# Optimization experiments

Measured on AMD Instinct MI355X. Metric: run time of the kernel, lower is better.

## Reference

```python
import math
import jax, jax.numpy as jnp
import numpy as np

H = 8  # h_heads (init kwarg)
D = 512  # d_hiddens
N, S = 4, 1024  # batch, seq (q == s assumed by the module's mask construction)
NEG = -1.0e9


def setup_inputs() -> dict:
    key = jax.random.key(0)
    ks = jax.random.split(key, 13)
    scale = 1.0 / math.sqrt(D)
    inp = {
        "queries_nqd": jax.random.normal(ks[0], (N, S, D), jnp.float32),
        "keys_nsd": jax.random.normal(ks[1], (N, S, D), jnp.float32),
        "values_nsd": jax.random.normal(ks[2], (N, S, D), jnp.float32),
        "prefix_len_n": jax.random.randint(ks[3], (N,), 0, S),
        "Wq": jax.random.normal(ks[4], (D, D), jnp.float32) * scale,
        "bq": jnp.zeros((D,), jnp.float32),
        "Wk": jax.random.normal(ks[5], (D, D), jnp.float32) * scale,
        "bk": jnp.zeros((D,), jnp.float32),
        "Wv": jax.random.normal(ks[6], (D, D), jnp.float32) * scale,
        "bv": jnp.zeros((D,), jnp.float32),
        "Wo": jax.random.normal(ks[7], (D, D), jnp.float32) * scale,
        "bo": jnp.zeros((D,), jnp.float32),
    }
    return inp


def _split_heads(x_nqd):
    n, q, d = x_nqd.shape
    return x_nqd.reshape(n, q, H, d // H).transpose(0, 2, 1, 3).reshape(n * H, q, d // H)


def _merge_heads(x_mqk):
    m, q, dh = x_mqk.shape
    return x_mqk.reshape(m // H, H, q, dh).transpose(0, 2, 1, 3).reshape(m // H, q, H * dh)


def reference(queries_nqd, keys_nsd, values_nsd, prefix_len_n, Wq, bq, Wk, bk, Wv, bv, Wo, bo):
    q_nqd = queries_nqd @ Wq.T + bq
    k_nsd = keys_nsd @ Wk.T + bk
    v_nsd = values_nsd @ Wv.T + bv

    q_mqk = _split_heads(q_nqd)   # [n*H, s, dh]
    k_msk = _split_heads(k_nsd)
    v_msk = _split_heads(v_nsd)
    prefix_m = jnp.repeat(prefix_len_n, H)  # per-head prefix, n-major to match split_heads

    dh = q_mqk.shape[-1]
    s = k_msk.shape[1]
    scores_mqs = jnp.einsum("mqd,msd->mqs", q_mqk, k_msk) / math.sqrt(dh)

    col = jnp.arange(s)
    block_mask = col[None, None, :] < prefix_m[:, None, None]        # [m,1,s] -> bcast [m,s,s]
    diag_mask = jnp.eye(s, dtype=bool)[None, :, :]                    # [1,s,s]
    attn_mask = block_mask | diag_mask                                # True = attend

    scores_mqs = jnp.where(attn_mask, scores_mqs, NEG)
    probs_mqs = jax.nn.softmax(scores_mqs, axis=-1)  # dropout p=0.0 -> identity
    out_mqk = jnp.einsum("mqs,msd->mqd", probs_mqs, v_msk)

    out_nqd = _merge_heads(out_mqk)
    return out_nqd @ Wo.T + bo
```

## Files before the change

kernel.cpp:

```cpp
#include <hip/hip_runtime.h>
#include <hip/hip_bf16.h>


typedef short bf16x8 __attribute__((ext_vector_type(8)));
typedef float f32x4 __attribute__((ext_vector_type(4)));
typedef int   i32x4 __attribute__((ext_vector_type(4)));
typedef unsigned short u16;
typedef unsigned int   u32;

#define MFMA_BF16(A, B, C) __builtin_amdgcn_mfma_f32_16x16x32_bf16((A), (B), (C), 0, 0, 0)

typedef const __attribute__((address_space(1))) void gv_t;
typedef __attribute__((address_space(3))) void lv_t;

__device__ __forceinline__ u16 cvt_bf16(float f) {
    return __builtin_bit_cast(u16, __float2bfloat16(f));
}
__device__ __forceinline__ u32 cvt2(float lo, float hi) {
    return (u32)cvt_bf16(lo) | ((u32)cvt_bf16(hi) << 16);
}

__global__ __launch_bounds__(256) void prep_kernel(
    const float* __restrict__ xq, const float* __restrict__ xk, const float* __restrict__ xv,
    const float* __restrict__ wq, const float* __restrict__ wk, const float* __restrict__ wv,
    const float* __restrict__ wo,
    u16* __restrict__ xqb, u16* __restrict__ xkb, u16* __restrict__ xvb,
    u16* __restrict__ wqb, u16* __restrict__ wkb, u16* __restrict__ wvb,
    u16* __restrict__ wob) {
    const int z = blockIdx.y;
    const float* src;
    u16* dst;
    int nblk;
    switch (z) {
        case 0: src = xq; dst = xqb; nblk = 1024; break;
        case 1: src = xk; dst = xkb; nblk = 1024; break;
        case 2: src = xv; dst = xvb; nblk = 1024; break;
        case 3: src = wq; dst = wqb; nblk = 128; break;
        case 4: src = wk; dst = wkb; nblk = 128; break;
        case 5: src = wv; dst = wvb; nblk = 128; break;
        default: src = wo; dst = wob; nblk = 128; break;
    }
    if (blockIdx.x >= (unsigned)nblk) return;
    size_t i = ((size_t)blockIdx.x * 256 + threadIdx.x) * 8;
    f32x4 a = *reinterpret_cast<const f32x4*>(src + i);
    f32x4 b = *reinterpret_cast<const f32x4*>(src + i + 4);
    i32x4 p;
    p[0] = cvt2(a[0], a[1]); p[1] = cvt2(a[2], a[3]);
    p[2] = cvt2(b[0], b[1]); p[3] = cvt2(b[2], b[3]);
    *reinterpret_cast<i32x4*>(dst + i) = p;
}

template <int OMODE>
__device__ __forceinline__ void gemm_bf(const u16* __restrict__ X,
                                        const u16* __restrict__ W,
                                        const float* __restrict__ bias,
                                        void* __restrict__ out_, float scale) {
    extern __shared__ char smem[];

    const int tid = threadIdx.x;
    const int m0 = blockIdx.x * 128;
    const int n0 = blockIdx.y * 64;
    const int w = tid >> 6, l = tid & 63;
    const int wm = (w >> 1) * 64, wn = (w & 1) * 32;
    const int lg = l >> 4, lr = l & 15;

    const int row8 = l >> 3;
    const int slotg = (l & 7) ^ row8;
    const u16* gA = X + (size_t)(m0 + w * 32 + row8) * 512 + slotg * 8;
    const u16* gB = W + (size_t)(n0 + w * 16 + row8) * 512 + slotg * 8;

    f32x4 acc[4][2];
#pragma unroll
    for (int i = 0; i < 4; i++)
#pragma unroll
        for (int j = 0; j < 2; j++) acc[i][j] = (f32x4){0.f, 0.f, 0.f, 0.f};

    auto STAGE = [&](int t, int buf) {
        char* As = smem + buf * 24576;
        char* Bs = As + 16384;
        const int k0 = t * 64;
#pragma unroll
        for (int c = 0; c < 4; c++)
            __builtin_amdgcn_global_load_lds((gv_t*)(gA + c * 8 * 512 + k0),
                                             (lv_t*)(As + (w * 4 + c) * 1024), 16, 0, 0);
#pragma unroll
        for (int c = 0; c < 2; c++)
            __builtin_amdgcn_global_load_lds((gv_t*)(gB + c * 8 * 512 + k0),
                                             (lv_t*)(Bs + (w * 2 + c) * 1024), 16, 0, 0);
    };
    auto COMPUTE = [&](int buf) {
        char* As = smem + buf * 24576;
        char* Bs = As + 16384;
#pragma unroll
        for (int kk = 0; kk < 2; kk++) {
            bf16x8 af[4], bfr[2];
#pragma unroll
            for (int i = 0; i < 4; i++) {
                int ra_ = wm + i * 16 + lr;
                af[i] = *reinterpret_cast<const bf16x8*>(
                    As + ra_ * 128 + ((kk * 64 + lg * 16) ^ ((ra_ & 7) << 4)));
            }
#pragma unroll
            for (int j = 0; j < 2; j++) {
                int rb_ = wn + j * 16 + lr;
                bfr[j] = *reinterpret_cast<const bf16x8*>(
                    Bs + rb_ * 128 + ((kk * 64 + lg * 16) ^ ((rb_ & 7) << 4)));
            }
            __builtin_amdgcn_s_setprio(1);
#pragma unroll
            for (int i = 0; i < 4; i++)
#pragma unroll
                for (int j = 0; j < 2; j++) acc[i][j] = MFMA_BF16(af[i], bfr[j], acc[i][j]);
            __builtin_amdgcn_s_setprio(0);
        }
    };

    STAGE(0, 0);
    __syncthreads();
    int buf = 0;
#pragma unroll
    for (int t = 0; t < 8; ++t) {
        if (t < 7) STAGE(t + 1, buf ^ 1);
        COMPUTE(buf);
        __syncthreads();
        buf ^= 1;
    }

#pragma unroll
    for (int j = 0; j < 2; j++) {
        int col = n0 + wn + j * 16 + lr;
        float bc_ = bias[col];
#pragma unroll
        for (int i = 0; i < 4; i++) {
            int grbase = m0 + wm + i * 16 + lg * 4;
            if (OMODE == 0) {
                float* out = (float*)out_;
#pragma unroll
                for (int r = 0; r < 4; r++)
                    out[(size_t)(grbase + r) * 512 + col] = (acc[i][j][r] + bc_) * scale;
            } else if (OMODE == 1) {
                u16* out = (u16*)out_;
#pragma unroll
                for (int r = 0; r < 4; r++)
                    out[(size_t)(grbase + r) * 512 + col] = cvt_bf16((acc[i][j][r] + bc_) * scale);
            } else {
                u16* out = (u16*)out_;
                int mh = ((grbase >> 10) * 8) + (col >> 6);
                int t2 = grbase & 1023;
                u32 p0 = cvt2((acc[i][j][0] + bc_) * scale, (acc[i][j][1] + bc_) * scale);
                u32 p1 = cvt2((acc[i][j][2] + bc_) * scale, (acc[i][j][3] + bc_) * scale);
                u32* dst = reinterpret_cast<u32*>(out + ((size_t)mh * 64 + (col & 63)) * 1024 + t2);
                dst[0] = p0;
                dst[1] = p1;
            }
        }
    }
}

__global__ __launch_bounds__(256) void qkv_gemm(
    const u16* __restrict__ Xq, const u16* __restrict__ Xk, const u16* __restrict__ Xv,
    const u16* __restrict__ Wq, const u16* __restrict__ Wk, const u16* __restrict__ Wv,
    const float* __restrict__ bq, const float* __restrict__ bk, const float* __restrict__ bv,
    u16* __restrict__ Qb, u16* __restrict__ Kb, u16* __restrict__ Vt) {
    int z = blockIdx.z;
    if (z == 0)      gemm_bf<1>(Xq, Wq, bq, Qb, 0.125f);
    else if (z == 1) gemm_bf<1>(Xk, Wk, bk, Kb, 1.0f);
    else             gemm_bf<2>(Xv, Wv, bv, Vt, 1.0f);
}

__global__ __launch_bounds__(256) void out_gemm(const u16* __restrict__ AO,
                                                const u16* __restrict__ Wo,
                                                const float* __restrict__ bo,
                                                float* __restrict__ out) {
    gemm_bf<0>(AO, Wo, bo, out, 1.0f);
}

__global__ __launch_bounds__(256) void attn_kernel(const u16* __restrict__ Qb,
                                                   const u16* __restrict__ Kb,
                                                   const u16* __restrict__ Vt,
                                                   const int* __restrict__ prefix,
                                                   u16* __restrict__ AO) {
    const int tid = threadIdx.x;
    const int w = tid >> 6, l = tid & 63;
    const int lg = l >> 4, lr = l & 15;
    const int qblk = blockIdx.x;
    const int m = blockIdx.y;
    const int n = m >> 3, h = m & 7;
    const int q0 = qblk * 64 + w * 16;
    const int P = prefix[n];

    const u16* qptr = Qb + (size_t)(n * 1024 + q0 + lr) * 512 + h * 64 + lg * 8;
    bf16x8 qf0 = *reinterpret_cast<const bf16x8*>(qptr);
    bf16x8 qf1 = *reinterpret_cast<const bf16x8*>(qptr + 32);

    f32x4 o[4];
#pragma unroll
    for (int j = 0; j < 4; j++) o[j] = (f32x4){0.f, 0.f, 0.f, 0.f};
    float mrow = -1.0e9f, lsum = 0.f;

    const int T = (P + 31) >> 5;
    const int dt = q0 >> 5;
    const int nt = T + ((dt >= T) ? 1 : 0);
    const int q_glob = q0 + lr;
    const f32x4 fz = (f32x4){0.f, 0.f, 0.f, 0.f};

    const u16* kbase = Kb + (size_t)(n * 1024 + lr) * 512 + h * 64 + lg * 8;
    const u16* vbase = Vt + ((size_t)m * 64 + lr) * 1024 + lg * 8;

    struct KV { bf16x8 k0, k1, k2, k3, v0, v1, v2, v3; };

    auto s0_of = [&](int it) { return ((it < T) ? it : dt) << 5; };
    auto LOADKV = [&](int s0, KV& t) {
        const u16* kp = kbase + (size_t)s0 * 512;
        t.k0 = *reinterpret_cast<const bf16x8*>(kp);
        t.k1 = *reinterpret_cast<const bf16x8*>(kp + 32);
        t.k2 = *reinterpret_cast<const bf16x8*>(kp + 16 * 512);
        t.k3 = *reinterpret_cast<const bf16x8*>(kp + 16 * 512 + 32);
        const u16* vp = vbase + s0;
        t.v0 = *reinterpret_cast<const bf16x8*>(vp);
        t.v1 = *reinterpret_cast<const bf16x8*>(vp + 16 * 1024);
        t.v2 = *reinterpret_cast<const bf16x8*>(vp + 32 * 1024);
        t.v3 = *reinterpret_cast<const bf16x8*>(vp + 48 * 1024);
    };
    auto STEP = [&](int s0, const KV& t) {
        f32x4 st[2];
        __builtin_amdgcn_s_setprio(1);
        st[0] = MFMA_BF16(t.k0, qf0, fz);
        st[0] = MFMA_BF16(t.k1, qf1, st[0]);
        st[1] = MFMA_BF16(t.k2, qf0, fz);
        st[1] = MFMA_BF16(t.k3, qf1, st[1]);
        __builtin_amdgcn_s_setprio(0);

        if (s0 + 32 > P) {
#pragma unroll
            for (int c = 0; c < 2; c++)
#pragma unroll
                for (int r = 0; r < 4; r++) {
                    int s = s0 + c * 16 + lg * 4 + r;
                    if (!((s < P) || (s == q_glob))) st[c][r] = -1.0e9f;
                }
        }

        float tm = st[0][0];
#pragma unroll
        for (int r = 1; r < 4; r++) tm = fmaxf(tm, st[0][r]);
#pragma unroll
        for (int r = 0; r < 4; r++) tm = fmaxf(tm, st[1][r]);
        tm = fmaxf(tm, __shfl_xor(tm, 16));
        tm = fmaxf(tm, __shfl_xor(tm, 32));

        const bool defer = __all(tm - mrow <= 8.0f);
        const float Mn = defer ? mrow : fmaxf(mrow, tm);

        float ts = 0.f;
#pragma unroll
        for (int c = 0; c < 2; c++)
#pragma unroll
            for (int r = 0; r < 4; r++) {
                float p = __expf(st[c][r] - Mn);
                st[c][r] = p;
                ts += p;
            }
        ts += __shfl_xor(ts, 16);
        ts += __shfl_xor(ts, 32);

        if (defer) {
            lsum += ts;
        } else {
            float alpha = __expf(mrow - Mn);
            lsum = lsum * alpha + ts;
            mrow = Mn;
            float a4[4];
#pragma unroll
            for (int r = 0; r < 4; r++) a4[r] = __shfl(alpha, lg * 4 + r);
#pragma unroll
            for (int j = 0; j < 4; j++) {
                o[j][0] *= a4[0]; o[j][1] *= a4[1]; o[j][2] *= a4[2]; o[j][3] *= a4[3];
            }
        }

        u32 pk[2][2];
#pragma unroll
        for (int c = 0; c < 2; c++) {
            pk[c][0] = cvt2(st[c][0], st[c][1]);
            pk[c][1] = cvt2(st[c][2], st[c][3]);
        }
        i32x4 pav;
#pragma unroll
        for (int wd = 0; wd < 4; wd++) {
            int src = ((2 * (lg & 1) + (wd >> 1)) << 4) + lr;
            int t0 = __shfl((int)pk[0][wd & 1], src);
            int t1 = __shfl((int)pk[1][wd & 1], src);
            pav[wd] = (lg >> 1) ? t1 : t0;
        }
        bf16x8 paf = __builtin_bit_cast(bf16x8, pav);

        __builtin_amdgcn_s_setprio(1);
        o[0] = MFMA_BF16(paf, t.v0, o[0]);
        o[1] = MFMA_BF16(paf, t.v1, o[1]);
        o[2] = MFMA_BF16(paf, t.v2, o[2]);
        o[3] = MFMA_BF16(paf, t.v3, o[3]);
        __builtin_amdgcn_s_setprio(0);
    };

    KV A_, B_;
    LOADKV(s0_of(0), A_);
    for (int it = 0; it < nt; it += 2) {
        if (it + 1 < nt) LOADKV(s0_of(it + 1), B_);
        STEP(s0_of(it), A_);
        if (it + 1 >= nt) break;
        if (it + 2 < nt) LOADKV(s0_of(it + 2), A_);
        STEP(s0_of(it + 1), B_);
    }

    float linv = 1.0f / fmaxf(lsum, 1.0e-30f);
    float li[4];
#pragma unroll
    for (int r = 0; r < 4; r++) li[r] = __shfl(linv, lg * 4 + r);

    u16* obase = AO + (size_t)(n * 1024 + q0 + lg * 4) * 512 + h * 64 + lr;
#pragma unroll
    for (int j = 0; j < 4; j++)
#pragma unroll
        for (int r = 0; r < 4; r++) {
            float v = fminf(fmaxf(o[j][r] * li[r], -1.0e4f), 1.0e4f);
            obase[(size_t)r * 512 + j * 16] = cvt_bf16(v);
        }
}

extern "C" void kernel_launch(void* const* d_in, const int* in_sizes, int n_in,
                              void* d_out, int out_size, void* d_ws, size_t ws_size,
                              hipStream_t stream) {
    (void)in_sizes; (void)n_in; (void)out_size;
    const float* queries = (const float*)d_in[0];
    const float* keys    = (const float*)d_in[1];
    const float* values  = (const float*)d_in[2];
    const int*   prefix  = (const int*)d_in[3];
    const float* Wq = (const float*)d_in[4];
    const float* bq = (const float*)d_in[5];
    const float* Wk = (const float*)d_in[6];
    const float* bk = (const float*)d_in[7];
    const float* Wv = (const float*)d_in[8];
    const float* bv = (const float*)d_in[9];
    const float* Wo = (const float*)d_in[10];
    const float* bo = (const float*)d_in[11];
    float* outp = (float*)d_out;

    const size_t XEL = (size_t)4096 * 512;
    const size_t WEL = (size_t)512 * 512;
    size_t need = (7 * XEL + 4 * WEL) * sizeof(u16);
    if (ws_size < need) return;
    u16* Xqb = (u16*)d_ws;
    u16* Xkb = Xqb + XEL;
    u16* Xvb = Xkb + XEL;
    u16* Wqb = Xvb + XEL;
    u16* Wkb = Wqb + WEL;
    u16* Wvb = Wkb + WEL;
    u16* Wob = Wvb + WEL;
    u16* Qb  = Wob + WEL;
    u16* Kb  = Qb + XEL;
    u16* Vt  = Kb + XEL;
    u16* AO  = Vt + XEL;

    dim3 blk(256);
    prep_kernel<<<dim3(1024, 7), blk, 0, stream>>>(queries, keys, values, Wq, Wk, Wv, Wo,
                                                   Xqb, Xkb, Xvb, Wqb, Wkb, Wvb, Wob);
    const int SMEM = 49152;
    qkv_gemm<<<dim3(32, 8, 3), blk, SMEM, stream>>>(Xqb, Xkb, Xvb, Wqb, Wkb, Wvb,
                                                    bq, bk, bv, Qb, Kb, Vt);
    attn_kernel<<<dim3(16, 32), blk, 0, stream>>>(Qb, Kb, Vt, prefix, AO);
    out_gemm<<<dim3(32, 8, 1), blk, SMEM, stream>>>(AO, Wob, bo, outp);
}
```

Baseline: 58.42 us.

## Fuse fp32-to-bf16 activation conversion into QKV GEMM A-tile loading

The QKV GEMM now reads the fp32 activations directly into registers, converts them to bf16 and writes them to LDS, overlapping with the MFMA compute of the previous tile. The prep kernel now converts only the four weight matrices, so the bf16 copies of the three large activation tensors are never written or read back, which removes that round trip through global memory. In exchange, A tiles go through registers instead of the direct global-to-LDS path, which raises register pressure and adds conversion work inside the GEMM. Each GEMM block also reads twice as many bytes of A from global memory.

```diff
diff --git a/kernel.cpp b/kernel.cpp
--- a/kernel.cpp
+++ b/kernel.cpp
@@ -21,26 +21,13 @@
 }
 
 __global__ __launch_bounds__(256) void prep_kernel(
-    const float* __restrict__ xq, const float* __restrict__ xk, const float* __restrict__ xv,
-    const float* __restrict__ wq, const float* __restrict__ wk, const float* __restrict__ wv,
-    const float* __restrict__ wo,
-    u16* __restrict__ xqb, u16* __restrict__ xkb, u16* __restrict__ xvb,
-    u16* __restrict__ wqb, u16* __restrict__ wkb, u16* __restrict__ wvb,
-    u16* __restrict__ wob) {
+    const float* __restrict__ wq, const float* __restrict__ wk,
+    const float* __restrict__ wv, const float* __restrict__ wo,
+    u16* __restrict__ wqb, u16* __restrict__ wkb,
+    u16* __restrict__ wvb, u16* __restrict__ wob) {
     const int z = blockIdx.y;
-    const float* src;
-    u16* dst;
-    int nblk;
-    switch (z) {
-        case 0: src = xq; dst = xqb; nblk = 1024; break;
-        case 1: src = xk; dst = xkb; nblk = 1024; break;
-        case 2: src = xv; dst = xvb; nblk = 1024; break;
-        case 3: src = wq; dst = wqb; nblk = 128; break;
-        case 4: src = wk; dst = wkb; nblk = 128; break;
-        case 5: src = wv; dst = wvb; nblk = 128; break;
-        default: src = wo; dst = wob; nblk = 128; break;
-    }
-    if (blockIdx.x >= (unsigned)nblk) return;
+    const float* src = (z == 0) ? wq : (z == 1) ? wk : (z == 2) ? wv : wo;
+    u16* dst = (z == 0) ? wqb : (z == 1) ? wkb : (z == 2) ? wvb : wob;
     size_t i = ((size_t)blockIdx.x * 256 + threadIdx.x) * 8;
     f32x4 a = *reinterpret_cast<const f32x4*>(src + i);
     f32x4 b = *reinterpret_cast<const f32x4*>(src + i + 4);
@@ -50,8 +37,8 @@
     *reinterpret_cast<i32x4*>(dst + i) = p;
 }
 
-template <int OMODE>
-__device__ __forceinline__ void gemm_bf(const u16* __restrict__ X,
+template <int AF32, int OMODE>
+__device__ __forceinline__ void gemm_bf(const void* __restrict__ X_,
                                         const u16* __restrict__ W,
                                         const float* __restrict__ bias,
                                         void* __restrict__ out_, float scale) {
@@ -66,26 +53,54 @@
 
     const int row8 = l >> 3;
     const int slotg = (l & 7) ^ row8;
-    const u16* gA = X + (size_t)(m0 + w * 32 + row8) * 512 + slotg * 8;
     const u16* gB = W + (size_t)(n0 + w * 16 + row8) * 512 + slotg * 8;
 
+    f32x4 ar[4][2];
+    const float* gAf = AF32 ? (const float*)X_ + (size_t)(m0 + w * 32 + row8) * 512 + slotg * 8
+                            : nullptr;
+    const u16* gAh = AF32 ? nullptr
+                          : (const u16*)X_ + (size_t)(m0 + w * 32 + row8) * 512 + slotg * 8;
+
     f32x4 acc[4][2];
 #pragma unroll
     for (int i = 0; i < 4; i++)
 #pragma unroll
         for (int j = 0; j < 2; j++) acc[i][j] = (f32x4){0.f, 0.f, 0.f, 0.f};
 
+    auto LOADA = [&](int t) {
+        const int k0 = t * 64;
+#pragma unroll
+        for (int c = 0; c < 4; c++) {
+            const float* ap = gAf + (size_t)c * 8 * 512 + k0;
+            ar[c][0] = *reinterpret_cast<const f32x4*>(ap);
+            ar[c][1] = *reinterpret_cast<const f32x4*>(ap + 4);
+        }
+    };
+    auto WRITEA = [&](int buf) {
+        char* As = smem + buf * 24576;
+#pragma unroll
+        for (int c = 0; c < 4; c++) {
+            i32x4 p;
+            p[0] = cvt2(ar[c][0][0], ar[c][0][1]);
+            p[1] = cvt2(ar[c][0][2], ar[c][0][3]);
+            p[2] = cvt2(ar[c][1][0], ar[c][1][1]);
+            p[3] = cvt2(ar[c][1][2], ar[c][1][3]);
+            *reinterpret_cast<i32x4*>(As + (w * 4 + c) * 1024 + l * 16) = p;
+        }
+    };
     auto STAGE = [&](int t, int buf) {
         char* As = smem + buf * 24576;
         char* Bs = As + 16384;
         const int k0 = t * 64;
-#pragma unroll
-        for (int c = 0; c < 4; c++)
-            __builtin_amdgcn_global_load_lds((gv_t*)(gA + c * 8 * 512 + k0),
-                                             (lv_t*)(As + (w * 4 + c) * 1024), 16, 0, 0);
+        if (!AF32) {
+#pragma unroll
+            for (int c = 0; c < 4; c++)
+                __builtin_amdgcn_global_load_lds((gv_t*)(gAh + (size_t)c * 8 * 512 + k0),
+                                                 (lv_t*)(As + (w * 4 + c) * 1024), 16, 0, 0);
+        }
 #pragma unroll
         for (int c = 0; c < 2; c++)
-            __builtin_amdgcn_global_load_lds((gv_t*)(gB + c * 8 * 512 + k0),
+            __builtin_amdgcn_global_load_lds((gv_t*)(gB + (size_t)c * 8 * 512 + k0),
                                              (lv_t*)(Bs + (w * 2 + c) * 1024), 16, 0, 0);
     };
     auto COMPUTE = [&](int buf) {
@@ -115,13 +130,18 @@
         }
     };
 
+    if (AF32) { LOADA(0); WRITEA(0); }
     STAGE(0, 0);
     __syncthreads();
     int buf = 0;
 #pragma unroll
     for (int t = 0; t < 8; ++t) {
-        if (t < 7) STAGE(t + 1, buf ^ 1);
+        if (t < 7) {
+            if (AF32) LOADA(t + 1);
+            STAGE(t + 1, buf ^ 1);
+        }
         COMPUTE(buf);
+        if (AF32 && t < 7) WRITEA(buf ^ 1);
         __syncthreads();
         buf ^= 1;
     }
@@ -158,21 +178,21 @@
 }
 
 __global__ __launch_bounds__(256) void qkv_gemm(
-    const u16* __restrict__ Xq, const u16* __restrict__ Xk, const u16* __restrict__ Xv,
+    const float* __restrict__ Xq, const float* __restrict__ Xk, const float* __restrict__ Xv,
     const u16* __restrict__ Wq, const u16* __restrict__ Wk, const u16* __restrict__ Wv,
     const float* __restrict__ bq, const float* __restrict__ bk, const float* __restrict__ bv,
     u16* __restrict__ Qb, u16* __restrict__ Kb, u16* __restrict__ Vt) {
     int z = blockIdx.z;
-    if (z == 0)      gemm_bf<1>(Xq, Wq, bq, Qb, 0.125f);
-    else if (z == 1) gemm_bf<1>(Xk, Wk, bk, Kb, 1.0f);
-    else             gemm_bf<2>(Xv, Wv, bv, Vt, 1.0f);
+    if (z == 0)      gemm_bf<1, 1>(Xq, Wq, bq, Qb, 0.125f);
+    else if (z == 1) gemm_bf<1, 1>(Xk, Wk, bk, Kb, 1.0f);
+    else             gemm_bf<1, 2>(Xv, Wv, bv, Vt, 1.0f);
 }
 
 __global__ __launch_bounds__(256) void out_gemm(const u16* __restrict__ AO,
                                                 const u16* __restrict__ Wo,
                                                 const float* __restrict__ bo,
                                                 float* __restrict__ out) {
-    gemm_bf<0>(AO, Wo, bo, out, 1.0f);
+    gemm_bf<0, 0>(AO, Wo, bo, out, 1.0f);
 }
 
 __global__ __launch_bounds__(256) void attn_kernel(const u16* __restrict__ Qb,
@@ -348,12 +368,9 @@
 
     const size_t XEL = (size_t)4096 * 512;
     const size_t WEL = (size_t)512 * 512;
-    size_t need = (7 * XEL + 4 * WEL) * sizeof(u16);
+    size_t need = (4 * WEL + 4 * XEL) * sizeof(u16);
     if (ws_size < need) return;
-    u16* Xqb = (u16*)d_ws;
-    u16* Xkb = Xqb + XEL;
-    u16* Xvb = Xkb + XEL;
-    u16* Wqb = Xvb + XEL;
+    u16* Wqb = (u16*)d_ws;
     u16* Wkb = Wqb + WEL;
     u16* Wvb = Wkb + WEL;
     u16* Wob = Wvb + WEL;
@@ -363,10 +380,9 @@
     u16* AO  = Vt + XEL;
 
     dim3 blk(256);
-    prep_kernel<<<dim3(1024, 7), blk, 0, stream>>>(queries, keys, values, Wq, Wk, Wv, Wo,
-                                                   Xqb, Xkb, Xvb, Wqb, Wkb, Wvb, Wob);
+    prep_kernel<<<dim3(128, 4), blk, 0, stream>>>(Wq, Wk, Wv, Wo, Wqb, Wkb, Wvb, Wob);
     const int SMEM = 49152;
-    qkv_gemm<<<dim3(32, 8, 3), blk, SMEM, stream>>>(Xqb, Xkb, Xvb, Wqb, Wkb, Wvb,
+    qkv_gemm<<<dim3(32, 8, 3), blk, SMEM, stream>>>(queries, keys, values, Wqb, Wkb, Wvb,
                                                     bq, bk, bv, Qb, Kb, Vt);
     attn_kernel<<<dim3(16, 32), blk, 0, stream>>>(Qb, Kb, Vt, prefix, AO);
     out_gemm<<<dim3(32, 8, 1), blk, SMEM, stream>>>(AO, Wob, bo, outp);
```

New measurement: 61.71 us. +5.6%, slower.
